# Optimization experiments

Measured on AMD Instinct MI355X. Metric: run time of the kernel, lower is better.

The kernel has to match this reference:

```python
import jax, jax.numpy as jnp
import numpy as np

B, T, C = 1, 4096, 1024   # batch, seq, n_embd
E, K = 64, 8              # num_experts, router top-k
G, TG = 8, 4              # n_group, topk_group
H, HS = 512, 2048         # expert hidden, shared-expert hidden
STD = 0.02


def setup_inputs() -> dict:
    key = jax.random.key(0)
    ks = jax.random.split(key, 9)
    return {
        "x": jax.random.normal(ks[0], (B, T, C), jnp.float32),
        "router_w": jax.random.normal(ks[1], (E, C), jnp.float32) * (C ** -0.5),
        "e_bias": jnp.zeros((E,), jnp.float32),  # e_score_correction_bias buffer
        "gate_w": jax.random.normal(ks[2], (E, C, H), jnp.float32) * STD,
        "up_w": jax.random.normal(ks[3], (E, C, H), jnp.float32) * STD,
        "down_w": jax.random.normal(ks[4], (E, H, C), jnp.float32) * STD,
        "sh_gate_w": jax.random.normal(ks[5], (C, HS), jnp.float32) * STD,
        "sh_up_w": jax.random.normal(ks[6], (C, HS), jnp.float32) * STD,
        "sh_down_w": jax.random.normal(ks[7], (HS, C), jnp.float32) * STD,
    }


def _route(xf, router_w, e_bias):
    # grouped sigmoid top-k routing with score-correction bias (group_limited_greedy)
    S = xf.shape[0]
    scores = jax.nn.sigmoid(xf @ router_w.T)          # [S,E], raw sigmoid scores
    sb = scores + e_bias                               # biased scores (selection only)
    epg = E // G
    # per-group score = sum of top (K // topk_group) biased scores in that group
    grp = jax.lax.top_k(sb.reshape(S, G, epg), K // TG)[0].sum(-1)   # [S,G]
    gidx = jax.lax.top_k(grp, TG)[1]                                 # [S,TG]
    gmask = jnp.zeros((S, G), bool).at[jnp.arange(S)[:, None], gidx].set(True)
    emask = jnp.repeat(gmask, epg, axis=1)                           # [S,E]
    masked = jnp.where(emask, sb, -jnp.inf)
    topk_idx = jax.lax.top_k(masked, K)[1]                           # [S,K]
    w = jnp.take_along_axis(scores, topk_idx, axis=1)                # raw scores gathered
    w = w / (w.sum(-1, keepdims=True) + 1e-20)                       # norm_topk_prob
    return topk_idx, w


def reference(x, router_w, e_bias, gate_w, up_w, down_w, sh_gate_w, sh_up_w, sh_down_w):
    Bq, Tq, Cq = x.shape
    xf = x.reshape(Bq * Tq, Cq)
    # always-on shared expert (SwiGLU)
    shared = (jax.nn.silu(xf @ sh_gate_w) * (xf @ sh_up_w)) @ sh_down_w
    topk_idx, w = _route(xf, router_w, e_bias)
    fe = topk_idx.reshape(-1)                          # [S*K] expert id per routed row
    order = jnp.argsort(fe, stable=True)               # sort rows by expert (grouped)
    tok = order // K                                   # source token of each sorted row
    sorted_x = xf[tok]                                 # [S*K, C]
    group_sizes = jnp.bincount(fe, length=E).astype(jnp.int32)
    # grouped GEMMs (== torch._grouped_mm / bmm-over-buckets in the original)
    g = jax.lax.ragged_dot(sorted_x, gate_w, group_sizes)
    u = jax.lax.ragged_dot(sorted_x, up_w, group_sizes)
    h = jax.nn.silu(g) * u
    o = jax.lax.ragged_dot(h, down_w, group_sizes)     # [S*K, C]
    o = o * w.reshape(-1)[order][:, None]              # weight by routing prob
    routed = jnp.zeros_like(xf).at[tok].add(o)         # combine back per token
    return (shared + routed).reshape(Bq, Tq, Cq)
```

## Files before the change

kernel.cpp:

```cpp
#include <hip/hip_runtime.h>
#include <hip/hip_bf16.h>
#include <stdint.h>


#define S_TOK 4096
#define C_DIM 1024
#define E_NUM 64
#define H_DIM 512
#define HS_DIM 2048
#define ROWS_TOTAL (S_TOK * 8)
#define T_TILES 320

typedef __attribute__((ext_vector_type(8))) short short8;
typedef __attribute__((ext_vector_type(4))) float f32x4;
typedef __attribute__((ext_vector_type(2))) unsigned int uint2v;

static __device__ __forceinline__ unsigned short f2bf(float f) {
    union { float f; uint32_t u; } v; v.f = f;
    uint32_t u = v.u;
    u += 0x7fffu + ((u >> 16) & 1u);
    return (unsigned short)(u >> 16);
}

static __device__ __forceinline__ void gl2lds16(const void* g, void* l) {
    __builtin_amdgcn_global_load_lds(
        (const __attribute__((address_space(1))) uint32_t*)g,
        (__attribute__((address_space(3))) uint32_t*)l, 16, 0, 0);
}

static __device__ __forceinline__ uint2v tr64(unsigned addr) {
    uint2v r;
    asm volatile("ds_read_b64_tr_b16 %0, %1" : "=v"(r) : "v"(addr));
    return r;
}

__global__ __launch_bounds__(256)
void router_scores_k(const float* __restrict__ x, const float* __restrict__ rw,
                     float* __restrict__ scores, int* __restrict__ counts) {
    if (blockIdx.x == 0 && threadIdx.x < E_NUM) counts[threadIdx.x] = 0;
    int t0 = blockIdx.x * 32;
    __shared__ float xs[32][36];
    __shared__ float wsm[64][36];
    int t = threadIdx.x;
    int tx = t & 15, ty = t >> 4;
    float acc[2][4] = {};
    for (int k0 = 0; k0 < C_DIM; k0 += 32) {
        {
            int r = t >> 3, c = t & 7;
            *(float4*)&xs[r][c * 4] = *(const float4*)(x + (size_t)(t0 + r) * C_DIM + k0 + c * 4);
        }
        #pragma unroll
        for (int i = 0; i < 2; i++) {
            int idx = t + 256 * i;
            int r = idx >> 3, c = idx & 7;
            *(float4*)&wsm[r][c * 4] = *(const float4*)(rw + (size_t)r * C_DIM + k0 + c * 4);
        }
        __syncthreads();
        #pragma unroll
        for (int kk = 0; kk < 32; kk += 4) {
            float4 a0 = *(const float4*)&xs[ty * 2 + 0][kk];
            float4 a1 = *(const float4*)&xs[ty * 2 + 1][kk];
            #pragma unroll
            for (int j = 0; j < 4; j++) {
                float4 b = *(const float4*)&wsm[tx * 4 + j][kk];
                acc[0][j] += a0.x * b.x + a0.y * b.y + a0.z * b.z + a0.w * b.w;
                acc[1][j] += a1.x * b.x + a1.y * b.y + a1.z * b.z + a1.w * b.w;
            }
        }
        __syncthreads();
    }
    #pragma unroll
    for (int i = 0; i < 2; i++)
        #pragma unroll
        for (int j = 0; j < 4; j++)
            scores[(size_t)(t0 + ty * 2 + i) * E_NUM + tx * 4 + j] =
                1.f / (1.f + __expf(-acc[i][j]));
}

__global__ __launch_bounds__(256)
void topk_k(const float* __restrict__ scores, const float* __restrict__ ebias,
            int* __restrict__ topk_idx, float* __restrict__ topk_w,
            int* __restrict__ counts) {
    int t = blockIdx.x * 4 + (threadIdx.x >> 6);
    int e = threadIdx.x & 63;
    float sc = scores[(size_t)t * E_NUM + e];
    float sb = sc + ebias[e];
    float m1 = sb, m2 = -1e30f;
    #pragma unroll
    for (int off = 1; off <= 4; off <<= 1) {
        float o1 = __shfl_xor(m1, off);
        float o2 = __shfl_xor(m2, off);
        float hi = fmaxf(m1, o1), lo = fminf(m1, o1);
        m2 = fmaxf(lo, fmaxf(m2, o2));
        m1 = hi;
    }
    float grp = m1 + m2;
    float grpv[8];
    #pragma unroll
    for (int g = 0; g < 8; g++) grpv[g] = __shfl(grp, g * 8);
    unsigned gsel = 0;
    #pragma unroll
    for (int k = 0; k < 4; k++) {
        float best = -1e30f; int bi = 0;
        #pragma unroll
        for (int g = 0; g < 8; g++)
            if (!((gsel >> g) & 1) && grpv[g] > best) { best = grpv[g]; bi = g; }
        gsel |= 1u << bi;
    }
    float val = ((gsel >> (e >> 3)) & 1) ? sb : -1e30f;
    int idx[8]; float sv[8]; float wsum = 0.f;
    #pragma unroll
    for (int k = 0; k < 8; k++) {
        uint32_t u = __float_as_uint(val);
        uint32_t mu = (u & 0x80000000u) ? ~u : (u | 0x80000000u);
        unsigned long long key = ((unsigned long long)mu << 6) | (unsigned long long)(63 - e);
        #pragma unroll
        for (int off = 32; off; off >>= 1) {
            unsigned long long ok = __shfl_xor(key, off);
            if (ok > key) key = ok;
        }
        int win = 63 - (int)(key & 63ull);
        idx[k] = win;
        sv[k] = __shfl(sc, win);
        wsum += sv[k];
        if (e == win) val = -1e30f;
    }
    float inv = 1.f / (wsum + 1e-20f);
    if (e < 8) {
        topk_idx[t * 8 + e] = idx[e];
        topk_w[t * 8 + e] = sv[e] * inv;
        atomicAdd(&counts[idx[e]], 1);
    }
}

__global__ void scan_k(const int* __restrict__ counts, int* __restrict__ base,
                       int* __restrict__ cursor, int* __restrict__ tile_e,
                       int* __restrict__ tile_m0) {
    int e = threadIdx.x;
    int c = counts[e];
    int s = c;
    #pragma unroll
    for (int off = 1; off < 64; off <<= 1) {
        int o = __shfl_up(s, off);
        if (e >= off) s += o;
    }
    int ex = s - c;
    base[e] = ex;
    cursor[e] = ex;
    int nt = (c + 127) >> 7;
    int ts = nt;
    #pragma unroll
    for (int off = 1; off < 64; off <<= 1) {
        int o = __shfl_up(ts, off);
        if (e >= off) ts += o;
    }
    int tb = ts - nt;
    for (int i = 0; i < nt; i++) { tile_e[tb + i] = e; tile_m0[tb + i] = i * 128; }
    int total = __shfl(ts, 63);
    for (int j = total + e; j < T_TILES; j += 64) tile_e[j] = -1;
}

__global__ void scatter_k(const int* __restrict__ topk_idx, const float* __restrict__ topk_w,
                          int* __restrict__ cursor, int* __restrict__ row_token,
                          float* __restrict__ row_wgt, int* __restrict__ pos_of) {
    int i = blockIdx.x * blockDim.x + threadIdx.x;
    int e = topk_idx[i];
    int pos = atomicAdd(&cursor[e], 1);
    row_token[pos] = i >> 3;
    row_wgt[pos] = topk_w[i];
    pos_of[i] = pos;
}

__global__ __launch_bounds__(256)
void combine_k(const float* __restrict__ O, const int* __restrict__ pos_of,
               float* __restrict__ out) {
    int t = blockIdx.x;
    int c = threadIdx.x;
    float4 s = ((const float4*)(out + (size_t)t * C_DIM))[c];
    int p[8];
    #pragma unroll
    for (int k = 0; k < 8; k++) p[k] = pos_of[t * 8 + k];
    #pragma unroll
    for (int k = 0; k < 8; k++) {
        float4 v = ((const float4*)(O + (size_t)p[k] * C_DIM))[c];
        s.x += v.x; s.y += v.y; s.z += v.z; s.w += v.w;
    }
    ((float4*)(out + (size_t)t * C_DIM))[c] = s;
}

__global__ void cvt_bf16_k(const float* __restrict__ in, unsigned short* __restrict__ out, int n8) {
    int i = blockIdx.x * blockDim.x + threadIdx.x;
    if (i >= n8) return;
    float4 v0 = ((const float4*)in)[2 * i];
    float4 v1 = ((const float4*)in)[2 * i + 1];
    unsigned short t[8] = { f2bf(v0.x), f2bf(v0.y), f2bf(v0.z), f2bf(v0.w),
                            f2bf(v1.x), f2bf(v1.y), f2bf(v1.z), f2bf(v1.w) };
    ((uint4*)out)[i] = *(uint4*)t;
}

template<bool FUSED, bool GATHER, bool WL, int EPI>
__global__ __launch_bounds__(256, 3)
void gemm2_k(const short* __restrict__ A, const short* __restrict__ B1b,
             const short* __restrict__ B2b, void* __restrict__ Cout,
             int M, int N, int K,
             const int* __restrict__ counts, const int* __restrict__ base,
             const int* __restrict__ row_token, const float* __restrict__ row_wgt,
             const int* __restrict__ tile_e, const int* __restrict__ tile_m0) {
    constexpr int BN = FUSED ? 64 : 128;
    constexpr int NJ = FUSED ? 2 : 4;
    constexpr int NC = BN / 16;
    constexpr int BS = BN * 32;

    int e = 0, m0, Mrows, rowbase = 0;
    if (WL) {
        e = tile_e[blockIdx.y];
        if (e < 0) return;
        m0 = tile_m0[blockIdx.y];
        Mrows = counts[e];
        rowbase = base[e];
    } else {
        m0 = blockIdx.y * 128;
        Mrows = M;
    }
    int n0 = blockIdx.x * BN;
    const short* B1 = B1b + (WL ? (size_t)e * N * K : 0);
    const short* B2 = FUSED ? (B2b + (WL ? (size_t)e * N * K : 0)) : nullptr;

    __shared__ short As[3 * 4096];
    __shared__ short Bs1[FUSED ? 3 * 2048 : 3 * 4096];
    __shared__ short Bs2[FUSED ? 3 * 2048 : 16];

    int tid = threadIdx.x;
    int lane = tid & 63, w = tid >> 6;
    int wr = w >> 1, wc = w & 1;
    int quad = lane >> 4, l16 = lane & 15;
    int sr = lane >> 2, sc = lane & 3;

    const short* aptr[2];
    #pragma unroll
    for (int i = 0; i < 2; i++) {
        int row = w * 32 + i * 16 + sr;
        int mrow = m0 + row;
        int cl = mrow < Mrows ? mrow : (Mrows - 1);
        size_t arow;
        if (GATHER)  arow = (size_t)row_token[rowbase + cl];
        else if (WL) arow = (size_t)(rowbase + cl);
        else         arow = (size_t)mrow;
        aptr[i] = A + arow * K + sc * 8;
    }

    const short* b1ptr[2];
    const short* b2ptr;
    {
        int L = lane;
        int r = (L & 7) >> 1, c = (L & 1) * 8;
        if constexpr (FUSED) {
            int kc = w * 2 + (L >> 5);
            int nc = (L >> 3) & 3;
            b1ptr[0] = B1 + (size_t)(kc * 4 + r) * N + n0 + nc * 16 + c;
            b2ptr    = B2 + (size_t)(kc * 4 + r) * N + n0 + nc * 16 + c;
        } else {
            int nc = L >> 3;
            #pragma unroll
            for (int i = 0; i < 2; i++) {
                int kc = w * 2 + i;
                b1ptr[i] = B1 + (size_t)(kc * 4 + r) * N + n0 + nc * 16 + c;
            }
            b2ptr = nullptr;
        }
    }

    f32x4 acc1[4][NJ] = {};
    f32x4 acc2[FUSED ? 4 : 1][NJ] = {};

    const int nk = K >> 5;
    auto stage = [&](int slot) {
        #pragma unroll
        for (int i = 0; i < 2; i++) {
            gl2lds16(aptr[i], &As[slot * 4096 + (w * 32 + i * 16) * 32]);
            aptr[i] += 32;
        }
        if constexpr (FUSED) {
            gl2lds16(b1ptr[0], &Bs1[slot * 2048 + w * 512]); b1ptr[0] += 32 * N;
            gl2lds16(b2ptr,    &Bs2[slot * 2048 + w * 512]); b2ptr += 32 * N;
        } else {
            #pragma unroll
            for (int i = 0; i < 2; i++) {
                gl2lds16(b1ptr[i], &Bs1[slot * 4096 + (w * 2 + i) * 512]);
                b1ptr[i] += 32 * N;
            }
        }
    };
    stage(0);
    if (nk > 1) stage(1);

    unsigned trb1 = (unsigned)(size_t)&Bs1[0] + (unsigned)(quad * 2 * NC * 128 + l16 * 8);
    unsigned trb2 = FUSED ? ((unsigned)(size_t)&Bs2[0] + (unsigned)(quad * 2 * NC * 128 + l16 * 8)) : 0u;
    auto rdB = [&](unsigned trb, int slot, int nb) -> short8 {
        unsigned a0 = trb + (unsigned)(slot * BS * 2 + nb * 128);
        uint2v lo = tr64(a0);
        uint2v hi = tr64(a0 + NC * 128);
        union { uint32_t u[4]; short8 s; } u;
        u.u[0] = lo[0]; u.u[1] = lo[1]; u.u[2] = hi[0]; u.u[3] = hi[1];
        return u.s;
    };

    int slot = 0, nslot = 2;
    for (int t = 0; t < nk; t++) {
        if (t + 1 < nk) {
            asm volatile("s_waitcnt vmcnt(4)" ::: "memory");
        } else {
            asm volatile("s_waitcnt vmcnt(0)" ::: "memory");
        }
        __builtin_amdgcn_s_barrier();
        __builtin_amdgcn_sched_barrier(0);

        if (t + 2 < nk) stage(nslot);

        short8 a[4], b1[NJ], b2[NJ];
        #pragma unroll
        for (int i = 0; i < 4; i++)
            a[i] = *(const short8*)&As[slot * 4096 + (wr * 64 + i * 16 + l16) * 32 + quad * 8];
        #pragma unroll
        for (int j = 0; j < NJ; j++) {
            int nb = wc * (BN / 32) + j;
            b1[j] = rdB(trb1, slot, nb);
            if constexpr (FUSED) b2[j] = rdB(trb2, slot, nb);
        }
        asm volatile("s_waitcnt lgkmcnt(0)" ::: "memory");
        __builtin_amdgcn_sched_barrier(0);
        #pragma unroll
        for (int i = 0; i < 4; i++)
            #pragma unroll
            for (int j = 0; j < NJ; j++) {
                acc1[i][j] = __builtin_amdgcn_mfma_f32_16x16x32_bf16(a[i], b1[j], acc1[i][j], 0, 0, 0);
                if (FUSED)
                    acc2[i][j] = __builtin_amdgcn_mfma_f32_16x16x32_bf16(a[i], b2[j], acc2[i][j], 0, 0, 0);
            }
        slot = (slot == 2) ? 0 : slot + 1;
        nslot = (nslot == 2) ? 0 : nslot + 1;
    }

    constexpr int CB = BN / 2;
    #pragma unroll
    for (int i = 0; i < 4; i++) {
        #pragma unroll
        for (int rr = 0; rr < 4; rr++) {
            int row = m0 + wr * 64 + i * 16 + quad * 4 + rr;
            if (row >= Mrows) continue;
            size_t orow = WL ? (size_t)(rowbase + row) : (size_t)row;
            float scl = 0.f;
            if (EPI == 2) scl = row_wgt[rowbase + row];
            #pragma unroll
            for (int j = 0; j < NJ; j++) {
                int n = n0 + wc * CB + j * 16 + l16;
                float v = acc1[i][j][rr];
                if (EPI == 0) {
                    float u = acc2[i][j][rr];
                    float h = v / (1.f + __expf(-v)) * u;
                    ((unsigned short*)Cout)[orow * N + n] = f2bf(h);
                } else if (EPI == 1) {
                    ((float*)Cout)[orow * N + n] = v;
                } else {
                    ((float*)Cout)[orow * N + n] = v * scl;
                }
            }
        }
    }
}

extern "C" void kernel_launch(void* const* d_in, const int* in_sizes, int n_in,
                              void* d_out, int out_size, void* d_ws, size_t ws_size,
                              hipStream_t stream) {
    const float* x        = (const float*)d_in[0];
    const float* router_w = (const float*)d_in[1];
    const float* e_bias   = (const float*)d_in[2];
    const float* gate_w   = (const float*)d_in[3];
    const float* up_w     = (const float*)d_in[4];
    const float* down_w   = (const float*)d_in[5];
    const float* sh_gate  = (const float*)d_in[6];
    const float* sh_up    = (const float*)d_in[7];
    const float* sh_down  = (const float*)d_in[8];
    float* out = (float*)d_out;
    char* ws = (char*)d_ws;

    int*   counts    = (int*)(ws);
    int*   base      = (int*)(ws + 256);
    int*   cursor    = (int*)(ws + 512);
    int*   topk_idx  = (int*)(ws + 1024);
    float* topk_w    = (float*)(ws + 1024 + 131072);
    int*   row_token = (int*)(ws + 1024 + 2 * 131072);
    float* row_wgt   = (float*)(ws + 1024 + 3 * 131072);
    float* scoresbuf = (float*)(ws + 1024 + 4 * 131072);
    int*   pos_of    = (int*)(ws + 1664 * 1024);
    int*   tile_e    = (int*)(ws + 1800 * 1024);
    int*   tile_m0   = (int*)(ws + 1808 * 1024);
    const size_t MB = 1u << 20;
    unsigned short* xb        = (unsigned short*)(ws + 2 * MB);
    unsigned short* Hs        = (unsigned short*)(ws + 10 * MB);
    unsigned short* Hr        = (unsigned short*)(ws + 26 * MB);
    unsigned short* sh_gate_b = (unsigned short*)(ws + 58 * MB);
    unsigned short* sh_up_b   = (unsigned short*)(ws + 62 * MB);
    unsigned short* sh_down_b = (unsigned short*)(ws + 66 * MB);
    unsigned short* gate_b    = (unsigned short*)(ws + 70 * MB);
    unsigned short* up_b      = (unsigned short*)(ws + 134 * MB);
    unsigned short* down_b    = (unsigned short*)(ws + 198 * MB);
    float* O = (float*)(ws + 70 * MB);

    router_scores_k<<<S_TOK / 32, 256, 0, stream>>>(x, router_w, scoresbuf, counts);
    topk_k<<<S_TOK / 4, 256, 0, stream>>>(scoresbuf, e_bias, topk_idx, topk_w, counts);
    scan_k<<<1, 64, 0, stream>>>(counts, base, cursor, tile_e, tile_m0);
    scatter_k<<<ROWS_TOTAL / 256, 256, 0, stream>>>(topk_idx, topk_w, cursor, row_token, row_wgt, pos_of);

    cvt_bf16_k<<<S_TOK * C_DIM / 8 / 256, 256, 0, stream>>>(x, xb, S_TOK * C_DIM / 8);
    const int NW = E_NUM * C_DIM * H_DIM / 8;
    cvt_bf16_k<<<NW / 256, 256, 0, stream>>>(gate_w, gate_b, NW);
    cvt_bf16_k<<<NW / 256, 256, 0, stream>>>(up_w,   up_b,   NW);
    cvt_bf16_k<<<NW / 256, 256, 0, stream>>>(down_w, down_b, NW);
    const int NS = C_DIM * HS_DIM / 8;
    cvt_bf16_k<<<NS / 256, 256, 0, stream>>>(sh_gate, sh_gate_b, NS);
    cvt_bf16_k<<<NS / 256, 256, 0, stream>>>(sh_up,   sh_up_b,   NS);
    cvt_bf16_k<<<NS / 256, 256, 0, stream>>>(sh_down, sh_down_b, NS);

    gemm2_k<true, false, false, 0><<<dim3(HS_DIM / 64, S_TOK / 128, 1), 256, 0, stream>>>(
        (const short*)xb, (const short*)sh_gate_b, (const short*)sh_up_b, Hs,
        S_TOK, HS_DIM, C_DIM, nullptr, nullptr, nullptr, nullptr, nullptr, nullptr);
    gemm2_k<false, false, false, 1><<<dim3(C_DIM / 128, S_TOK / 128, 1), 256, 0, stream>>>(
        (const short*)Hs, (const short*)sh_down_b, nullptr, out,
        S_TOK, C_DIM, HS_DIM, nullptr, nullptr, nullptr, nullptr, nullptr, nullptr);

    gemm2_k<true, true, true, 0><<<dim3(H_DIM / 64, T_TILES, 1), 256, 0, stream>>>(
        (const short*)xb, (const short*)gate_b, (const short*)up_b, Hr,
        0, H_DIM, C_DIM, counts, base, row_token, row_wgt, tile_e, tile_m0);
    gemm2_k<false, false, true, 2><<<dim3(C_DIM / 128, T_TILES, 1), 256, 0, stream>>>(
        (const short*)Hr, (const short*)down_b, nullptr, O,
        0, C_DIM, H_DIM, counts, base, row_token, row_wgt, tile_e, tile_m0);

    combine_k<<<S_TOK, 256, 0, stream>>>(O, pos_of, out);
}
```

Before: 943.5 us.

## Merge conversion launches and co-schedule shared and routed expert GEMMs

```diff
diff --git a/kernel.cpp b/kernel.cpp
--- a/kernel.cpp
+++ b/kernel.cpp
@@ -10,6 +10,10 @@
 #define HS_DIM 2048
 #define ROWS_TOTAL (S_TOK * 8)
 #define T_TILES 320
+#define NB_ROUTED_F (T_TILES * 8)
+#define NB_SHARED_F (32 * 32)
+#define NB_ROUTED_D (T_TILES * 8)
+#define NB_SHARED_D (32 * 8)
 
 typedef __attribute__((ext_vector_type(8))) short short8;
 typedef __attribute__((ext_vector_type(4))) float f32x4;
@@ -188,47 +192,75 @@
     ((float4*)(out + (size_t)t * C_DIM))[c] = s;
 }
 
-__global__ void cvt_bf16_k(const float* __restrict__ in, unsigned short* __restrict__ out, int n8) {
-    int i = blockIdx.x * blockDim.x + threadIdx.x;
-    if (i >= n8) return;
-    float4 v0 = ((const float4*)in)[2 * i];
-    float4 v1 = ((const float4*)in)[2 * i + 1];
+__global__ __launch_bounds__(256)
+void cvt_all_k(const float* __restrict__ i0, unsigned short* __restrict__ o0, int n0,
+               const float* __restrict__ i1, unsigned short* __restrict__ o1, int n1,
+               const float* __restrict__ i2, unsigned short* __restrict__ o2, int n2,
+               const float* __restrict__ i3, unsigned short* __restrict__ o3, int n3,
+               const float* __restrict__ i4, unsigned short* __restrict__ o4, int n4,
+               const float* __restrict__ i5, unsigned short* __restrict__ o5, int n5,
+               const float* __restrict__ i6, unsigned short* __restrict__ o6, int n6) {
+    int g = blockIdx.x * 256 + threadIdx.x;
+    const float* in; unsigned short* out;
+    if (g < n0) { in = i0; out = o0; }
+    else { g -= n0;
+    if (g < n1) { in = i1; out = o1; }
+    else { g -= n1;
+    if (g < n2) { in = i2; out = o2; }
+    else { g -= n2;
+    if (g < n3) { in = i3; out = o3; }
+    else { g -= n3;
+    if (g < n4) { in = i4; out = o4; }
+    else { g -= n4;
+    if (g < n5) { in = i5; out = o5; }
+    else { g -= n5;
+    if (g >= n6) return;
+    in = i6; out = o6; } } } } } }
+    float4 v0 = ((const float4*)in)[2 * g];
+    float4 v1 = ((const float4*)in)[2 * g + 1];
     unsigned short t[8] = { f2bf(v0.x), f2bf(v0.y), f2bf(v0.z), f2bf(v0.w),
                             f2bf(v1.x), f2bf(v1.y), f2bf(v1.z), f2bf(v1.w) };
-    ((uint4*)out)[i] = *(uint4*)t;
-}
-
-template<bool FUSED, bool GATHER, bool WL, int EPI>
+    ((uint4*)out)[g] = *(uint4*)t;
+}
+
 __global__ __launch_bounds__(256, 3)
-void gemm2_k(const short* __restrict__ A, const short* __restrict__ B1b,
-             const short* __restrict__ B2b, void* __restrict__ Cout,
-             int M, int N, int K,
-             const int* __restrict__ counts, const int* __restrict__ base,
-             const int* __restrict__ row_token, const float* __restrict__ row_wgt,
-             const int* __restrict__ tile_e, const int* __restrict__ tile_m0) {
-    constexpr int BN = FUSED ? 64 : 128;
-    constexpr int NJ = FUSED ? 2 : 4;
-    constexpr int NC = BN / 16;
-    constexpr int BS = BN * 32;
-
-    int e = 0, m0, Mrows, rowbase = 0;
-    if (WL) {
-        e = tile_e[blockIdx.y];
+void fused_all_k(const short* __restrict__ xb,
+                 const short* __restrict__ gate_b, const short* __restrict__ up_b,
+                 const short* __restrict__ shg_b, const short* __restrict__ shu_b,
+                 unsigned short* __restrict__ Hr, unsigned short* __restrict__ Hs,
+                 const int* __restrict__ counts, const int* __restrict__ base,
+                 const int* __restrict__ row_token,
+                 const int* __restrict__ tile_e, const int* __restrict__ tile_m0) {
+    constexpr int K = C_DIM;
+    constexpr int NC = 4;
+    constexpr int BS = 64 * 32;
+
+    int bid = blockIdx.x;
+    bool routed = bid < NB_ROUTED_F;
+    const short* B1; const short* B2; unsigned short* Cout;
+    int m0, n0, Mrows, rowbase, N;
+    if (routed) {
+        int ti = bid >> 3;
+        int e = tile_e[ti];
         if (e < 0) return;
-        m0 = tile_m0[blockIdx.y];
-        Mrows = counts[e];
-        rowbase = base[e];
+        m0 = tile_m0[ti]; n0 = (bid & 7) * 64;
+        Mrows = counts[e]; rowbase = base[e];
+        N = H_DIM;
+        B1 = gate_b + (size_t)e * H_DIM * K;
+        B2 = up_b   + (size_t)e * H_DIM * K;
+        Cout = Hr;
     } else {
-        m0 = blockIdx.y * 128;
-        Mrows = M;
-    }
-    int n0 = blockIdx.x * BN;
-    const short* B1 = B1b + (WL ? (size_t)e * N * K : 0);
-    const short* B2 = FUSED ? (B2b + (WL ? (size_t)e * N * K : 0)) : nullptr;
+        int s = bid - NB_ROUTED_F;
+        m0 = (s >> 5) * 128; n0 = (s & 31) * 64;
+        Mrows = S_TOK; rowbase = 0;
+        N = HS_DIM;
+        B1 = shg_b; B2 = shu_b;
+        Cout = Hs;
+    }
 
     __shared__ short As[3 * 4096];
-    __shared__ short Bs1[FUSED ? 3 * 2048 : 3 * 4096];
-    __shared__ short Bs2[FUSED ? 3 * 2048 : 16];
+    __shared__ short Bs1[3 * BS / 2 * 2];
+    __shared__ short Bs2[3 * 2048];
 
     int tid = threadIdx.x;
     int lane = tid & 63, w = tid >> 6;
@@ -242,36 +274,24 @@
         int row = w * 32 + i * 16 + sr;
         int mrow = m0 + row;
         int cl = mrow < Mrows ? mrow : (Mrows - 1);
-        size_t arow;
-        if (GATHER)  arow = (size_t)row_token[rowbase + cl];
-        else if (WL) arow = (size_t)(rowbase + cl);
-        else         arow = (size_t)mrow;
-        aptr[i] = A + arow * K + sc * 8;
-    }
-
-    const short* b1ptr[2];
+        size_t arow = routed ? (size_t)row_token[rowbase + cl] : (size_t)cl;
+        aptr[i] = xb + arow * K + sc * 8;
+    }
+
+    const short* b1ptr;
     const short* b2ptr;
     {
         int L = lane;
         int r = (L & 7) >> 1, c = (L & 1) * 8;
-        if constexpr (FUSED) {
-            int kc = w * 2 + (L >> 5);
-            int nc = (L >> 3) & 3;
-            b1ptr[0] = B1 + (size_t)(kc * 4 + r) * N + n0 + nc * 16 + c;
-            b2ptr    = B2 + (size_t)(kc * 4 + r) * N + n0 + nc * 16 + c;
-        } else {
-            int nc = L >> 3;
-            #pragma unroll
-            for (int i = 0; i < 2; i++) {
-                int kc = w * 2 + i;
-                b1ptr[i] = B1 + (size_t)(kc * 4 + r) * N + n0 + nc * 16 + c;
-            }
-            b2ptr = nullptr;
-        }
-    }
-
-    f32x4 acc1[4][NJ] = {};
-    f32x4 acc2[FUSED ? 4 : 1][NJ] = {};
+        int kc = w * 2 + (L >> 5);
+        int nc = (L >> 3) & 3;
+        b1ptr = B1 + (size_t)(kc * 4 + r) * N + n0 + nc * 16 + c;
+        b2ptr = B2 + (size_t)(kc * 4 + r) * N + n0 + nc * 16 + c;
+    }
+    const size_t bstep = (size_t)32 * N;
+
+    f32x4 acc1[4][2] = {};
+    f32x4 acc2[4][2] = {};
 
     const int nk = K >> 5;
     auto stage = [&](int slot) {
@@ -280,24 +300,16 @@
             gl2lds16(aptr[i], &As[slot * 4096 + (w * 32 + i * 16) * 32]);
             aptr[i] += 32;
         }
-        if constexpr (FUSED) {
-            gl2lds16(b1ptr[0], &Bs1[slot * 2048 + w * 512]); b1ptr[0] += 32 * N;
-            gl2lds16(b2ptr,    &Bs2[slot * 2048 + w * 512]); b2ptr += 32 * N;
-        } else {
-            #pragma unroll
-            for (int i = 0; i < 2; i++) {
-                gl2lds16(b1ptr[i], &Bs1[slot * 4096 + (w * 2 + i) * 512]);
-                b1ptr[i] += 32 * N;
-            }
-        }
+        gl2lds16(b1ptr, &Bs1[slot * 2048 + w * 512]); b1ptr += bstep;
+        gl2lds16(b2ptr, &Bs2[slot * 2048 + w * 512]); b2ptr += bstep;
     };
     stage(0);
-    if (nk > 1) stage(1);
+    stage(1);
 
     unsigned trb1 = (unsigned)(size_t)&Bs1[0] + (unsigned)(quad * 2 * NC * 128 + l16 * 8);
-    unsigned trb2 = FUSED ? ((unsigned)(size_t)&Bs2[0] + (unsigned)(quad * 2 * NC * 128 + l16 * 8)) : 0u;
+    unsigned trb2 = (unsigned)(size_t)&Bs2[0] + (unsigned)(quad * 2 * NC * 128 + l16 * 8);
     auto rdB = [&](unsigned trb, int slot, int nb) -> short8 {
-        unsigned a0 = trb + (unsigned)(slot * BS * 2 + nb * 128);
+        unsigned a0 = trb + (unsigned)(slot * 4096 + nb * 128);
         uint2v lo = tr64(a0);
         uint2v hi = tr64(a0 + NC * 128);
         union { uint32_t u[4]; short8 s; } u;
@@ -317,53 +329,184 @@
 
         if (t + 2 < nk) stage(nslot);
 
-        short8 a[4], b1[NJ], b2[NJ];
+        short8 a[4], b1[2], b2[2];
         #pragma unroll
         for (int i = 0; i < 4; i++)
             a[i] = *(const short8*)&As[slot * 4096 + (wr * 64 + i * 16 + l16) * 32 + quad * 8];
         #pragma unroll
-        for (int j = 0; j < NJ; j++) {
-            int nb = wc * (BN / 32) + j;
+        for (int j = 0; j < 2; j++) {
+            int nb = wc * 2 + j;
             b1[j] = rdB(trb1, slot, nb);
-            if constexpr (FUSED) b2[j] = rdB(trb2, slot, nb);
+            b2[j] = rdB(trb2, slot, nb);
         }
         asm volatile("s_waitcnt lgkmcnt(0)" ::: "memory");
         __builtin_amdgcn_sched_barrier(0);
         #pragma unroll
         for (int i = 0; i < 4; i++)
             #pragma unroll
-            for (int j = 0; j < NJ; j++) {
+            for (int j = 0; j < 2; j++) {
                 acc1[i][j] = __builtin_amdgcn_mfma_f32_16x16x32_bf16(a[i], b1[j], acc1[i][j], 0, 0, 0);
-                if (FUSED)
-                    acc2[i][j] = __builtin_amdgcn_mfma_f32_16x16x32_bf16(a[i], b2[j], acc2[i][j], 0, 0, 0);
+                acc2[i][j] = __builtin_amdgcn_mfma_f32_16x16x32_bf16(a[i], b2[j], acc2[i][j], 0, 0, 0);
             }
         slot = (slot == 2) ? 0 : slot + 1;
         nslot = (nslot == 2) ? 0 : nslot + 1;
     }
 
-    constexpr int CB = BN / 2;
     #pragma unroll
     for (int i = 0; i < 4; i++) {
         #pragma unroll
         for (int rr = 0; rr < 4; rr++) {
             int row = m0 + wr * 64 + i * 16 + quad * 4 + rr;
             if (row >= Mrows) continue;
-            size_t orow = WL ? (size_t)(rowbase + row) : (size_t)row;
-            float scl = 0.f;
-            if (EPI == 2) scl = row_wgt[rowbase + row];
+            size_t orow = (size_t)(rowbase + row);
             #pragma unroll
-            for (int j = 0; j < NJ; j++) {
-                int n = n0 + wc * CB + j * 16 + l16;
+            for (int j = 0; j < 2; j++) {
+                int n = n0 + wc * 32 + j * 16 + l16;
                 float v = acc1[i][j][rr];
-                if (EPI == 0) {
-                    float u = acc2[i][j][rr];
-                    float h = v / (1.f + __expf(-v)) * u;
-                    ((unsigned short*)Cout)[orow * N + n] = f2bf(h);
-                } else if (EPI == 1) {
-                    ((float*)Cout)[orow * N + n] = v;
-                } else {
-                    ((float*)Cout)[orow * N + n] = v * scl;
-                }
+                float u = acc2[i][j][rr];
+                float h = v / (1.f + __expf(-v)) * u;
+                Cout[orow * N + n] = f2bf(h);
+            }
+        }
+    }
+}
+
+__global__ __launch_bounds__(256, 3)
+void down_all_k(const short* __restrict__ Hr, const short* __restrict__ Hs,
+                const short* __restrict__ down_b, const short* __restrict__ shd_b,
+                float* __restrict__ O, float* __restrict__ out,
+                const int* __restrict__ counts, const int* __restrict__ base,
+                const float* __restrict__ row_wgt,
+                const int* __restrict__ tile_e, const int* __restrict__ tile_m0) {
+    constexpr int N = C_DIM;
+    constexpr int NC = 8;
+    constexpr int BS = 128 * 32;
+
+    int bid = blockIdx.x;
+    bool routed = bid < NB_ROUTED_D;
+    const short* A; const short* B1; float* Cout;
+    int m0, n0, Mrows, rowbase, K;
+    if (routed) {
+        int ti = bid >> 3;
+        int e = tile_e[ti];
+        if (e < 0) return;
+        m0 = tile_m0[ti]; n0 = (bid & 7) * 128;
+        Mrows = counts[e]; rowbase = base[e];
+        K = H_DIM;
+        A = Hr;
+        B1 = down_b + (size_t)e * N * H_DIM;
+        Cout = O;
+    } else {
+        int s = bid - NB_ROUTED_D;
+        m0 = (s >> 3) * 128; n0 = (s & 7) * 128;
+        Mrows = S_TOK; rowbase = 0;
+        K = HS_DIM;
+        A = Hs;
+        B1 = shd_b;
+        Cout = out;
+    }
+
+    __shared__ short As[3 * 4096];
+    __shared__ short Bs1[3 * BS];
+
+    int tid = threadIdx.x;
+    int lane = tid & 63, w = tid >> 6;
+    int wr = w >> 1, wc = w & 1;
+    int quad = lane >> 4, l16 = lane & 15;
+    int sr = lane >> 2, sc = lane & 3;
+
+    const short* aptr[2];
+    #pragma unroll
+    for (int i = 0; i < 2; i++) {
+        int row = w * 32 + i * 16 + sr;
+        int mrow = m0 + row;
+        int cl = mrow < Mrows ? mrow : (Mrows - 1);
+        aptr[i] = A + (size_t)(rowbase + cl) * K + sc * 8;
+    }
+
+    const short* b1ptr[2];
+    {
+        int L = lane;
+        int r = (L & 7) >> 1, c = (L & 1) * 8;
+        int nc = L >> 3;
+        #pragma unroll
+        for (int i = 0; i < 2; i++) {
+            int kc = w * 2 + i;
+            b1ptr[i] = B1 + (size_t)(kc * 4 + r) * N + n0 + nc * 16 + c;
+        }
+    }
+    const size_t bstep = (size_t)32 * N;
+
+    f32x4 acc1[4][4] = {};
+
+    const int nk = K >> 5;
+    auto stage = [&](int slot) {
+        #pragma unroll
+        for (int i = 0; i < 2; i++) {
+            gl2lds16(aptr[i], &As[slot * 4096 + (w * 32 + i * 16) * 32]);
+            aptr[i] += 32;
+        }
+        #pragma unroll
+        for (int i = 0; i < 2; i++) {
+            gl2lds16(b1ptr[i], &Bs1[slot * BS + (w * 2 + i) * 512]);
+            b1ptr[i] += bstep;
+        }
+    };
+    stage(0);
+    stage(1);
+
+    unsigned trb1 = (unsigned)(size_t)&Bs1[0] + (unsigned)(quad * 2 * NC * 128 + l16 * 8);
+    auto rdB = [&](int slot, int nb) -> short8 {
+        unsigned a0 = trb1 + (unsigned)(slot * BS * 2 + nb * 128);
+        uint2v lo = tr64(a0);
+        uint2v hi = tr64(a0 + NC * 128);
+        union { uint32_t u[4]; short8 s; } u;
+        u.u[0] = lo[0]; u.u[1] = lo[1]; u.u[2] = hi[0]; u.u[3] = hi[1];
+        return u.s;
+    };
+
+    int slot = 0, nslot = 2;
+    for (int t = 0; t < nk; t++) {
+        if (t + 1 < nk) {
+            asm volatile("s_waitcnt vmcnt(4)" ::: "memory");
+        } else {
+            asm volatile("s_waitcnt vmcnt(0)" ::: "memory");
+        }
+        __builtin_amdgcn_s_barrier();
+        __builtin_amdgcn_sched_barrier(0);
+
+        if (t + 2 < nk) stage(nslot);
+
+        short8 a[4], b1[4];
+        #pragma unroll
+        for (int i = 0; i < 4; i++)
+            a[i] = *(const short8*)&As[slot * 4096 + (wr * 64 + i * 16 + l16) * 32 + quad * 8];
+        #pragma unroll
+        for (int j = 0; j < 4; j++)
+            b1[j] = rdB(slot, wc * 4 + j);
+        asm volatile("s_waitcnt lgkmcnt(0)" ::: "memory");
+        __builtin_amdgcn_sched_barrier(0);
+        #pragma unroll
+        for (int i = 0; i < 4; i++)
+            #pragma unroll
+            for (int j = 0; j < 4; j++)
+                acc1[i][j] = __builtin_amdgcn_mfma_f32_16x16x32_bf16(a[i], b1[j], acc1[i][j], 0, 0, 0);
+        slot = (slot == 2) ? 0 : slot + 1;
+        nslot = (nslot == 2) ? 0 : nslot + 1;
+    }
+
+    #pragma unroll
+    for (int i = 0; i < 4; i++) {
+        #pragma unroll
+        for (int rr = 0; rr < 4; rr++) {
+            int row = m0 + wr * 64 + i * 16 + quad * 4 + rr;
+            if (row >= Mrows) continue;
+            size_t orow = (size_t)(rowbase + row);
+            float scl = routed ? row_wgt[rowbase + row] : 1.f;
+            #pragma unroll
+            for (int j = 0; j < 4; j++) {
+                int n = n0 + wc * 64 + j * 16 + l16;
+                Cout[orow * N + n] = acc1[i][j][rr] * scl;
             }
         }
     }
@@ -412,29 +555,22 @@
     scan_k<<<1, 64, 0, stream>>>(counts, base, cursor, tile_e, tile_m0);
     scatter_k<<<ROWS_TOTAL / 256, 256, 0, stream>>>(topk_idx, topk_w, cursor, row_token, row_wgt, pos_of);
 
-    cvt_bf16_k<<<S_TOK * C_DIM / 8 / 256, 256, 0, stream>>>(x, xb, S_TOK * C_DIM / 8);
+    const int NX = S_TOK * C_DIM / 8;
     const int NW = E_NUM * C_DIM * H_DIM / 8;
-    cvt_bf16_k<<<NW / 256, 256, 0, stream>>>(gate_w, gate_b, NW);
-    cvt_bf16_k<<<NW / 256, 256, 0, stream>>>(up_w,   up_b,   NW);
-    cvt_bf16_k<<<NW / 256, 256, 0, stream>>>(down_w, down_b, NW);
     const int NS = C_DIM * HS_DIM / 8;
-    cvt_bf16_k<<<NS / 256, 256, 0, stream>>>(sh_gate, sh_gate_b, NS);
-    cvt_bf16_k<<<NS / 256, 256, 0, stream>>>(sh_up,   sh_up_b,   NS);
-    cvt_bf16_k<<<NS / 256, 256, 0, stream>>>(sh_down, sh_down_b, NS);
-
-    gemm2_k<true, false, false, 0><<<dim3(HS_DIM / 64, S_TOK / 128, 1), 256, 0, stream>>>(
-        (const short*)xb, (const short*)sh_gate_b, (const short*)sh_up_b, Hs,
-        S_TOK, HS_DIM, C_DIM, nullptr, nullptr, nullptr, nullptr, nullptr, nullptr);
-    gemm2_k<false, false, false, 1><<<dim3(C_DIM / 128, S_TOK / 128, 1), 256, 0, stream>>>(
-        (const short*)Hs, (const short*)sh_down_b, nullptr, out,
-        S_TOK, C_DIM, HS_DIM, nullptr, nullptr, nullptr, nullptr, nullptr, nullptr);
-
-    gemm2_k<true, true, true, 0><<<dim3(H_DIM / 64, T_TILES, 1), 256, 0, stream>>>(
-        (const short*)xb, (const short*)gate_b, (const short*)up_b, Hr,
-        0, H_DIM, C_DIM, counts, base, row_token, row_wgt, tile_e, tile_m0);
-    gemm2_k<false, false, true, 2><<<dim3(C_DIM / 128, T_TILES, 1), 256, 0, stream>>>(
-        (const short*)Hr, (const short*)down_b, nullptr, O,
-        0, C_DIM, H_DIM, counts, base, row_token, row_wgt, tile_e, tile_m0);
+    const int NTOT = NX + 3 * NW + 3 * NS;
+    cvt_all_k<<<(NTOT + 255) / 256, 256, 0, stream>>>(
+        x, xb, NX, gate_w, gate_b, NW, up_w, up_b, NW, down_w, down_b, NW,
+        sh_gate, sh_gate_b, NS, sh_up, sh_up_b, NS, sh_down, sh_down_b, NS);
+
+    fused_all_k<<<NB_ROUTED_F + NB_SHARED_F, 256, 0, stream>>>(
+        (const short*)xb, (const short*)gate_b, (const short*)up_b,
+        (const short*)sh_gate_b, (const short*)sh_up_b, Hr, Hs,
+        counts, base, row_token, tile_e, tile_m0);
+
+    down_all_k<<<NB_ROUTED_D + NB_SHARED_D, 256, 0, stream>>>(
+        (const short*)Hr, (const short*)Hs, (const short*)down_b, (const short*)sh_down_b,
+        O, out, counts, base, row_wgt, tile_e, tile_m0);
 
     combine_k<<<S_TOK, 256, 0, stream>>>(O, pos_of, out);
 }
```

New measurement: 917.0 us. 1.03x faster.
